# Kernel tuning notes

Measured on AMD Instinct MI355X. Metric: run time of the kernel, lower is better.

Reference implementation:

```python
import jax, jax.numpy as jnp
import numpy as np

NUM_HEADS = 16

def setup_inputs() -> dict:
    key = jax.random.key(0)
    ks = jax.random.split(key, 5)
    B, T, C = 2, 2048, 1024
    s = 0.02
    return {
        "x": jax.random.normal(ks[0], (B, T, C), dtype=jnp.float32),
        "in_w": jax.random.normal(ks[1], (3 * C, C), dtype=jnp.float32) * s,
        "in_b": jax.random.normal(ks[2], (3 * C,), dtype=jnp.float32) * s,
        "out_w": jax.random.normal(ks[3], (C, C), dtype=jnp.float32) * s,
        "out_b": jax.random.normal(ks[4], (C,), dtype=jnp.float32) * s,
    }

def reference(x, in_w, in_b, out_w, out_b):
    B, T, C = x.shape
    H = NUM_HEADS
    D = C // H
    qvk = x @ in_w.T + in_b  # (B, T, 3C)
    # einops 'b t (d k h) -> k b h t d': factor 3C as (D, 3, H), D outermost
    qvk = qvk.reshape(B, T, D, 3, H).transpose(3, 0, 4, 1, 2)  # (3, B, H, T, D)
    q, v, k = qvk[0], qvk[1], qvk[2]  # note q, v, k assignment order
    scores = jnp.einsum('bhid,bhjd->bhij', q, k) * (D ** -0.5)  # (B, H, T, T)
    causal = jnp.tril(jnp.ones((T, T), dtype=bool))
    scores = jnp.where(causal, scores, -jnp.inf)
    attn = jax.nn.softmax(scores, axis=-1)
    out = jnp.einsum('bhij,bhjd->bhid', attn, v)  # (B, H, T, D)
    out = out.transpose(0, 2, 1, 3).reshape(B, T, C)  # 'b h t d -> b t (h d)'
    return out @ out_w.T + out_b
```

## Files before the change

kernel.cpp:

```cpp
#include <hip/hip_runtime.h>


#define BB 2
#define TT 2048
#define CC 1024
#define HH 16
#define DD 64
#define MM (BB*TT)
#define N3 (3*CC)
#define BH (BB*HH)

typedef unsigned short u16;
typedef unsigned int   u32;
typedef __bf16 bf16x8 __attribute__((ext_vector_type(8)));
typedef float  f32x4  __attribute__((ext_vector_type(4)));

__device__ __forceinline__ u16 f32_to_bf16(float f) {
  u32 u = __float_as_uint(f);
  return (u16)((u + 0x7fffu + ((u >> 16) & 1u)) >> 16);
}
__device__ __forceinline__ u16 f32_to_bf16_fast(float f) {
  return (u16)((__float_as_uint(f) + 0x8000u) >> 16);
}
__device__ __forceinline__ u32 pack2_bf16(float a, float b) {
  u32 ua = __float_as_uint(a) + 0x8000u;
  u32 ub = __float_as_uint(b) + 0x8000u;
  return __builtin_amdgcn_perm(ub, ua, 0x07060302);
}

#define N4_X  (MM * CC / 4)
#define N4_W  (N3 * CC / 4)
#define N4_OW (CC * CC / 4)
__global__ __launch_bounds__(256) void cast_all(const float* __restrict__ x,
                                                const float* __restrict__ in_w,
                                                const float* __restrict__ out_w,
                                                u16* __restrict__ xb,
                                                u16* __restrict__ wb,
                                                u16* __restrict__ owb) {
  int i = blockIdx.x * 256 + threadIdx.x;
  const float* src; u16* dst; int j;
  if (i < N4_X)            { src = x;     dst = xb;  j = i; }
  else if (i < N4_X + N4_W){ src = in_w;  dst = wb;  j = i - N4_X; }
  else                     { src = out_w; dst = owb; j = i - N4_X - N4_W; }
  float4 f = reinterpret_cast<const float4*>(src)[j];
  uint2 pk;
  pk.x = (u32)f32_to_bf16(f.x) | ((u32)f32_to_bf16(f.y) << 16);
  pk.y = (u32)f32_to_bf16(f.z) | ((u32)f32_to_bf16(f.w) << 16);
  reinterpret_cast<uint2*>(dst)[j] = pk;
}

__device__ __forceinline__ void gemm_core(const u16* __restrict__ Ag,
                                          const u16* __restrict__ Bg,
                                          int K, u16* Al, u16* Bl,
                                          int m0, int n0, f32x4 acc[4][4]) {
  const int tid = threadIdx.x, lane = tid & 63, w = tid >> 6;
  const int quad = lane >> 4, colr = lane & 15;
  const int mw = (w >> 1) * 64, nw = (w & 1) * 64;
  const int srow = lane >> 3, scol = lane & 7;
  const uint4* Al4 = reinterpret_cast<const uint4*>(Al);
  const uint4* Bl4 = reinterpret_cast<const uint4*>(Bl);
  for (int kt = 0; kt < K / 64; ++kt) {
    __syncthreads();
    #pragma unroll
    for (int ii = 0; ii < 4; ++ii) {
      int inst = w * 4 + ii;
      int row = inst * 8 + srow;
      int cs = scol ^ (row & 7);
      const u16* ga = Ag + (size_t)(m0 + row) * K + kt * 64 + cs * 8;
      const u16* gb = Bg + (size_t)(n0 + row) * K + kt * 64 + cs * 8;
      __builtin_amdgcn_global_load_lds(
          (const __attribute__((address_space(1))) void*)ga,
          (__attribute__((address_space(3))) void*)(Al + inst * 512), 16, 0, 0);
      __builtin_amdgcn_global_load_lds(
          (const __attribute__((address_space(1))) void*)gb,
          (__attribute__((address_space(3))) void*)(Bl + inst * 512), 16, 0, 0);
    }
    __syncthreads();
    #pragma unroll
    for (int ks = 0; ks < 2; ++ks) {
      bf16x8 af[4], bfr[4];
      #pragma unroll
      for (int t = 0; t < 4; ++t) {
        int mrow = mw + t * 16 + colr;
        af[t]  = __builtin_bit_cast(bf16x8, Al4[mrow * 8 + ((ks * 4 + quad) ^ (mrow & 7))]);
        int nrow = nw + t * 16 + colr;
        bfr[t] = __builtin_bit_cast(bf16x8, Bl4[nrow * 8 + ((ks * 4 + quad) ^ (nrow & 7))]);
      }
      #pragma unroll
      for (int mt = 0; mt < 4; ++mt)
        #pragma unroll
        for (int nt = 0; nt < 4; ++nt)
          acc[mt][nt] = __builtin_amdgcn_mfma_f32_16x16x32_bf16(af[mt], bfr[nt], acc[mt][nt], 0, 0, 0);
    }
  }
}

__global__ __launch_bounds__(256) void gemm_qkv(const u16* __restrict__ xb,
                                                const u16* __restrict__ wb,
                                                const float* __restrict__ in_b,
                                                u16* __restrict__ Y) {
  __shared__ __align__(16) u16 Al[128 * 64];
  __shared__ __align__(16) u16 Bl[128 * 64];
  const int lane = threadIdx.x & 63, w = threadIdx.x >> 6;
  const int quad = lane >> 4, colr = lane & 15;
  const int mw = (w >> 1) * 64, nw = (w & 1) * 64;
  const int m0 = blockIdx.x * 128, n0 = blockIdx.y * 128;
  f32x4 acc[4][4];
  #pragma unroll
  for (int mt = 0; mt < 4; ++mt)
    #pragma unroll
    for (int nt = 0; nt < 4; ++nt) acc[mt][nt] = (f32x4){0.f, 0.f, 0.f, 0.f};
  gemm_core(xb, wb, CC, Al, Bl, m0, n0, acc);
  float bias[4];
  #pragma unroll
  for (int nt = 0; nt < 4; ++nt) bias[nt] = in_b[n0 + nw + nt * 16 + colr];
  #pragma unroll
  for (int mt = 0; mt < 4; ++mt)
    #pragma unroll
    for (int e = 0; e < 4; ++e) {
      int row = m0 + mw + mt * 16 + quad * 4 + e;
      #pragma unroll
      for (int nt = 0; nt < 4; ++nt)
        Y[(size_t)row * N3 + n0 + nw + nt * 16 + colr] = f32_to_bf16(acc[mt][nt][e] + bias[nt]);
    }
}

__global__ __launch_bounds__(256) void repack_qkv(const u16* __restrict__ Y,
                                                  u16* __restrict__ qkv) {
  __shared__ __align__(16) u16 Yl[N3];
  const int m = blockIdx.x, tid = threadIdx.x;
  const int b_ = m >> 11, t = m & (TT - 1);
  const uint4* Yg = reinterpret_cast<const uint4*>(Y + (size_t)m * N3);
  uint4* Yl4 = reinterpret_cast<uint4*>(Yl);
  for (int i = tid; i < N3 / 8; i += 256) Yl4[i] = Yg[i];
  __syncthreads();
  for (int it = tid; it < 768; it += 256) {
    int h = it & 15, s = (it >> 4) % 3, dg = it / 48;
    int col = s * 16 + h;
    u32 lo = (u32)Yl[(dg * 4 + 0) * 48 + col] | ((u32)Yl[(dg * 4 + 1) * 48 + col] << 16);
    u32 hi = (u32)Yl[(dg * 4 + 2) * 48 + col] | ((u32)Yl[(dg * 4 + 3) * 48 + col] << 16);
    uint2 pk; pk.x = lo; pk.y = hi;
    size_t base = (((size_t)s * BH + b_ * HH + h) * TT + t) * DD + dg * 4;
    *reinterpret_cast<uint2*>(qkv + base) = pk;
  }
}

__global__ __launch_bounds__(128) void attn_mfma(const u16* __restrict__ qkv,
                                                 u16* __restrict__ aout) {
  __shared__ __align__(16) u32   Vt[2][64 * 36];
  __shared__ __align__(16) float Pl[2 * 32 * 68];
  const int tid  = threadIdx.x;
  const int lane = tid & 63, w = tid >> 6;
  const int quad = lane >> 4, colr = lane & 15;
  const int flat = blockIdx.x;
  const int bh = (flat & 7) * 4 + (flat >> 7);
  const int pr = (flat >> 3) & 15;
  const int b_ = bh >> 4, h = bh & 15;

  const uint4* Qg4 = reinterpret_cast<const uint4*>(qkv + (size_t)bh * TT * DD);
  const uint4* Vg4 = reinterpret_cast<const uint4*>(qkv + ((size_t)BH + bh) * TT * DD);
  const uint4* Kg4 = reinterpret_cast<const uint4*>(qkv + ((size_t)2 * BH + bh) * TT * DD);
  const float4* Pl4 = reinterpret_cast<const float4*>(Pl);

  const int s_jp = tid & 31, s_half = tid >> 5;
  const int wbase = w * (32 * 68);

  for (int pass = 0; pass < 2; ++pass) {
    const int qt = pass ? (31 - pr) : pr;
    const int i0 = qt * 64;
    const int jmax = qt;

    bf16x8 qa[2][2];
    #pragma unroll
    for (int u = 0; u < 2; ++u)
      #pragma unroll
      for (int ks = 0; ks < 2; ++ks)
        qa[u][ks] = __builtin_bit_cast(bf16x8,
            Qg4[(size_t)(i0 + w * 32 + u * 16 + colr) * 8 + ks * 4 + quad]);

    f32x4 oacc[2][4];
    #pragma unroll
    for (int u = 0; u < 2; ++u)
      #pragma unroll
      for (int dt = 0; dt < 4; ++dt) oacc[u][dt] = (f32x4){0.f, 0.f, 0.f, 0.f};
    float lp[2] = {0.f, 0.f};

    uint4 va[2], vb[2];
    #pragma unroll
    for (int io = 0; io < 2; ++io) {
      va[io] = Vg4[(size_t)(2 * s_jp) * 8 + s_half + io * 4];
      vb[io] = Vg4[(size_t)(2 * s_jp + 1) * 8 + s_half + io * 4];
    }

    for (int jt = 0; jt <= jmax; ++jt) {
      const int j0 = jt * 64;
      u32* vtw = Vt[jt & 1];
      const uint4* vt4 = reinterpret_cast<const uint4*>(Vt[jt & 1]);

      uint4 kraw[4][2];
      #pragma unroll
      for (int t4 = 0; t4 < 4; ++t4)
        #pragma unroll
        for (int ks = 0; ks < 2; ++ks)
          kraw[t4][ks] = Kg4[(size_t)(j0 + t4 * 16 + colr) * 8 + ks * 4 + quad];

      #pragma unroll
      for (int io = 0; io < 2; ++io) {
        const int oc = s_half + io * 4;
        u32 aw[4] = {va[io].x, va[io].y, va[io].z, va[io].w};
        u32 bw[4] = {vb[io].x, vb[io].y, vb[io].z, vb[io].w};
        #pragma unroll
        for (int m = 0; m < 4; ++m) {
          vtw[(oc * 8 + 2 * m)     * 36 + s_jp] = __builtin_amdgcn_perm(bw[m], aw[m], 0x05040100);
          vtw[(oc * 8 + 2 * m + 1) * 36 + s_jp] = __builtin_amdgcn_perm(bw[m], aw[m], 0x07060302);
        }
      }
      if (jt < jmax) {
        int nj = j0 + 64;
        #pragma unroll
        for (int io = 0; io < 2; ++io) {
          va[io] = Vg4[(size_t)(nj + 2 * s_jp) * 8 + s_half + io * 4];
          vb[io] = Vg4[(size_t)(nj + 2 * s_jp + 1) * 8 + s_half + io * 4];
        }
      }
      __syncthreads();

      f32x4 sacc[2][4];
      #pragma unroll
      for (int u = 0; u < 2; ++u)
        #pragma unroll
        for (int t4 = 0; t4 < 4; ++t4) sacc[u][t4] = (f32x4){0.f, 0.f, 0.f, 0.f};
      #pragma unroll
      for (int t4 = 0; t4 < 4; ++t4)
        #pragma unroll
        for (int ks = 0; ks < 2; ++ks) {
          bf16x8 kb = __builtin_bit_cast(bf16x8, kraw[t4][ks]);
          #pragma unroll
          for (int u = 0; u < 2; ++u)
            sacc[u][t4] = __builtin_amdgcn_mfma_f32_16x16x32_bf16(qa[u][ks], kb, sacc[u][t4], 0, 0, 0);
        }

      const bool maskt = (jt == qt);
      #pragma unroll
      for (int u = 0; u < 2; ++u)
        #pragma unroll
        for (int t4 = 0; t4 < 4; ++t4)
          #pragma unroll
          for (int rg = 0; rg < 4; ++rg) {
            float p = __builtin_amdgcn_exp2f(sacc[u][t4][rg] * 0.18033688011112042f);
            if (maskt && (t4 * 16 + colr > w * 32 + u * 16 + quad * 4 + rg)) p = 0.f;
            Pl[wbase + (u * 16 + quad * 4 + rg) * 68 + t4 * 16 + colr] = p;
          }

      bf16x8 pa[2][2];
      #pragma unroll
      for (int u = 0; u < 2; ++u)
        #pragma unroll
        for (int ks = 0; ks < 2; ++ks) {
          int b4 = (wbase + (u * 16 + colr) * 68 + ks * 32 + quad * 8) >> 2;
          float4 f0 = Pl4[b4], f1 = Pl4[b4 + 1];
          lp[u] += ((f0.x + f0.y) + (f0.z + f0.w)) + ((f1.x + f1.y) + (f1.z + f1.w));
          uint4 up;
          up.x = pack2_bf16(f0.x, f0.y); up.y = pack2_bf16(f0.z, f0.w);
          up.z = pack2_bf16(f1.x, f1.y); up.w = pack2_bf16(f1.z, f1.w);
          pa[u][ks] = __builtin_bit_cast(bf16x8, up);
        }

      #pragma unroll
      for (int dt = 0; dt < 4; ++dt)
        #pragma unroll
        for (int ks = 0; ks < 2; ++ks) {
          bf16x8 vfr = __builtin_bit_cast(bf16x8, vt4[(dt * 16 + colr) * 9 + ks * 4 + quad]);
          #pragma unroll
          for (int u = 0; u < 2; ++u)
            oacc[u][dt] = __builtin_amdgcn_mfma_f32_16x16x32_bf16(pa[u][ks], vfr, oacc[u][dt], 0, 0, 0);
        }
    }

    #pragma unroll
    for (int u = 0; u < 2; ++u) {
      float ls = lp[u];
      ls += __shfl_xor(ls, 16);
      ls += __shfl_xor(ls, 32);
      float linv[4];
      #pragma unroll
      for (int rg = 0; rg < 4; ++rg)
        linv[rg] = 1.0f / __shfl(ls, quad * 4 + rg);
      #pragma unroll
      for (int dt = 0; dt < 4; ++dt)
        #pragma unroll
        for (int rg = 0; rg < 4; ++rg) {
          int ig = i0 + w * 32 + u * 16 + quad * 4 + rg;
          size_t off = ((size_t)(b_ * TT + ig)) * CC + h * DD + dt * 16 + colr;
          aout[off] = f32_to_bf16_fast(oacc[u][dt][rg] * linv[rg]);
        }
    }
    __syncthreads();
  }
}

__global__ __launch_bounds__(256) void gemm_out(const u16* __restrict__ ab,
                                                const u16* __restrict__ owb,
                                                const float* __restrict__ out_b,
                                                float* __restrict__ out) {
  __shared__ __align__(16) u16 Al[128 * 64];
  __shared__ __align__(16) u16 Bl[128 * 64];
  const int lane = threadIdx.x & 63, w = threadIdx.x >> 6;
  const int quad = lane >> 4, colr = lane & 15;
  const int mw = (w >> 1) * 64, nw = (w & 1) * 64;
  const int m0 = blockIdx.x * 128, n0 = blockIdx.y * 128;
  f32x4 acc[4][4];
  #pragma unroll
  for (int mt = 0; mt < 4; ++mt)
    #pragma unroll
    for (int nt = 0; nt < 4; ++nt) acc[mt][nt] = (f32x4){0.f, 0.f, 0.f, 0.f};
  gemm_core(ab, owb, CC, Al, Bl, m0, n0, acc);
  float bias[4];
  #pragma unroll
  for (int nt = 0; nt < 4; ++nt) bias[nt] = out_b[n0 + nw + nt * 16 + colr];
  #pragma unroll
  for (int mt = 0; mt < 4; ++mt)
    #pragma unroll
    for (int e = 0; e < 4; ++e) {
      int row = m0 + mw + mt * 16 + quad * 4 + e;
      #pragma unroll
      for (int nt = 0; nt < 4; ++nt)
        out[(size_t)row * CC + n0 + nw + nt * 16 + colr] = acc[mt][nt][e] + bias[nt];
    }
}

extern "C" void kernel_launch(void* const* d_in, const int* in_sizes, int n_in,
                              void* d_out, int out_size, void* d_ws, size_t ws_size,
                              hipStream_t stream) {
  const float* x     = (const float*)d_in[0];
  const float* in_w  = (const float*)d_in[1];
  const float* in_b  = (const float*)d_in[2];
  const float* out_w = (const float*)d_in[3];
  const float* out_b = (const float*)d_in[4];
  float* out = (float*)d_out;

  char* ws = (char*)d_ws;
  u16* xb  = (u16*)(ws + 0);
  u16* ab  = (u16*)(ws + 0);
  u16* wb  = (u16*)(ws + 8388608);
  u16* owb = (u16*)(ws + 14680064);
  u16* Y   = (u16*)(ws + 16777216);
  u16* qkv = (u16*)(ws + 41943040);

  cast_all<<<dim3((N4_X + N4_W + N4_OW) / 256), 256, 0, stream>>>(x, in_w, out_w, xb, wb, owb);

  gemm_qkv<<<dim3(MM / 128, N3 / 128), 256, 0, stream>>>(xb, wb, in_b, Y);
  repack_qkv<<<dim3(MM), 256, 0, stream>>>(Y, qkv);
  attn_mfma<<<dim3(512), 128, 0, stream>>>(qkv, ab);
  gemm_out<<<dim3(MM / 128, CC / 128), 256, 0, stream>>>(ab, owb, out_b, out);
}
```

Before: 226.2 us.

## Fuse QKV repack into GEMM epilogue and split attention KV range across blocks

Permutes in_w rows during the cast so the QKV GEMM writes directly in head-major layout, with the softmax scale folded into the K columns, which removes the repack kernel and the intermediate Y buffer. Attention now splits each query-tile pair's key range into four chunks across 2048 blocks and accumulates unnormalized outputs and row sums with float atomics. A new finalize kernel then normalizes the results and writes bf16. P is packed to bf16 in LDS, the Vt buffer is single-buffered, and K loads are moved inside the loop. This buys more parallelism at the cost of a large memset, atomic traffic and an extra pass.

New measurement: 246.4 us. 1.09x slower.

```diff
diff --git a/kernel.cpp b/kernel.cpp
--- a/kernel.cpp
+++ b/kernel.cpp
@@ -9,6 +9,7 @@
 #define MM (BB*TT)
 #define N3 (3*CC)
 #define BH (BB*HH)
+#define KSCALE 0.18033688011112042f
 
 typedef unsigned short u16;
 typedef unsigned int   u32;
@@ -18,9 +19,6 @@
 __device__ __forceinline__ u16 f32_to_bf16(float f) {
   u32 u = __float_as_uint(f);
   return (u16)((u + 0x7fffu + ((u >> 16) & 1u)) >> 16);
-}
-__device__ __forceinline__ u16 f32_to_bf16_fast(float f) {
-  return (u16)((__float_as_uint(f) + 0x8000u) >> 16);
 }
 __device__ __forceinline__ u32 pack2_bf16(float a, float b) {
   u32 ua = __float_as_uint(a) + 0x8000u;
@@ -38,11 +36,14 @@
                                                 u16* __restrict__ wb,
                                                 u16* __restrict__ owb) {
   int i = blockIdx.x * 256 + threadIdx.x;
-  const float* src; u16* dst; int j;
-  if (i < N4_X)            { src = x;     dst = xb;  j = i; }
-  else if (i < N4_X + N4_W){ src = in_w;  dst = wb;  j = i - N4_X; }
-  else                     { src = out_w; dst = owb; j = i - N4_X - N4_W; }
-  float4 f = reinterpret_cast<const float4*>(src)[j];
+  const float* src; u16* dst; int j; int sj;
+  if (i < N4_X)             { src = x;     dst = xb;  j = i;               sj = j; }
+  else if (i < N4_X + N4_W) { src = in_w;  dst = wb;  j = i - N4_X;
+                              int rp = j >> 8, c = j & 255;
+                              int s = rp >> 10, h = (rp >> 6) & 15, d = rp & 63;
+                              sj = (d * 48 + s * 16 + h) * 256 + c; }
+  else                      { src = out_w; dst = owb; j = i - N4_X - N4_W; sj = j; }
+  float4 f = reinterpret_cast<const float4*>(src)[sj];
   uint2 pk;
   pk.x = (u32)f32_to_bf16(f.x) | ((u32)f32_to_bf16(f.y) << 16);
   pk.y = (u32)f32_to_bf16(f.z) | ((u32)f32_to_bf16(f.w) << 16);
@@ -98,7 +99,7 @@
 __global__ __launch_bounds__(256) void gemm_qkv(const u16* __restrict__ xb,
                                                 const u16* __restrict__ wb,
                                                 const float* __restrict__ in_b,
-                                                u16* __restrict__ Y) {
+                                                u16* __restrict__ qkv) {
   __shared__ __align__(16) u16 Al[128 * 64];
   __shared__ __align__(16) u16 Bl[128 * 64];
   const int lane = threadIdx.x & 63, w = threadIdx.x >> 6;
@@ -111,64 +112,57 @@
     #pragma unroll
     for (int nt = 0; nt < 4; ++nt) acc[mt][nt] = (f32x4){0.f, 0.f, 0.f, 0.f};
   gemm_core(xb, wb, CC, Al, Bl, m0, n0, acc);
-  float bias[4];
-  #pragma unroll
-  for (int nt = 0; nt < 4; ++nt) bias[nt] = in_b[n0 + nw + nt * 16 + colr];
-  #pragma unroll
-  for (int mt = 0; mt < 4; ++mt)
-    #pragma unroll
-    for (int e = 0; e < 4; ++e) {
-      int row = m0 + mw + mt * 16 + quad * 4 + e;
-      #pragma unroll
-      for (int nt = 0; nt < 4; ++nt)
-        Y[(size_t)row * N3 + n0 + nw + nt * 16 + colr] = f32_to_bf16(acc[mt][nt][e] + bias[nt]);
-    }
-}
-
-__global__ __launch_bounds__(256) void repack_qkv(const u16* __restrict__ Y,
-                                                  u16* __restrict__ qkv) {
-  __shared__ __align__(16) u16 Yl[N3];
-  const int m = blockIdx.x, tid = threadIdx.x;
-  const int b_ = m >> 11, t = m & (TT - 1);
-  const uint4* Yg = reinterpret_cast<const uint4*>(Y + (size_t)m * N3);
-  uint4* Yl4 = reinterpret_cast<uint4*>(Yl);
-  for (int i = tid; i < N3 / 8; i += 256) Yl4[i] = Yg[i];
-  __syncthreads();
-  for (int it = tid; it < 768; it += 256) {
-    int h = it & 15, s = (it >> 4) % 3, dg = it / 48;
-    int col = s * 16 + h;
-    u32 lo = (u32)Yl[(dg * 4 + 0) * 48 + col] | ((u32)Yl[(dg * 4 + 1) * 48 + col] << 16);
-    u32 hi = (u32)Yl[(dg * 4 + 2) * 48 + col] | ((u32)Yl[(dg * 4 + 3) * 48 + col] << 16);
-    uint2 pk; pk.x = lo; pk.y = hi;
-    size_t base = (((size_t)s * BH + b_ * HH + h) * TT + t) * DD + dg * 4;
-    *reinterpret_cast<uint2*>(qkv + base) = pk;
+  const int b_ = m0 >> 11;
+  #pragma unroll
+  for (int nt = 0; nt < 4; ++nt) {
+    int np = n0 + nw + nt * 16 + colr;
+    int s = np >> 10, h = (np >> 6) & 15, d = np & 63;
+    float bias = in_b[d * 48 + s * 16 + h];
+    float sc = (s == 2) ? KSCALE : 1.0f;
+    u16* base = qkv + ((size_t)(s * BH + b_ * HH + h) * TT) * DD + d;
+    #pragma unroll
+    for (int mt = 0; mt < 4; ++mt)
+      #pragma unroll
+      for (int e = 0; e < 4; ++e) {
+        int t = (m0 + mw + mt * 16 + quad * 4 + e) & (TT - 1);
+        base[(size_t)t * DD] = f32_to_bf16((acc[mt][nt][e] + bias) * sc);
+      }
   }
 }
 
-__global__ __launch_bounds__(128) void attn_mfma(const u16* __restrict__ qkv,
-                                                 u16* __restrict__ aout) {
-  __shared__ __align__(16) u32   Vt[2][64 * 36];
-  __shared__ __align__(16) float Pl[2 * 32 * 68];
+__global__ __launch_bounds__(128, 4) void attn_mfma(const u16* __restrict__ qkv,
+                                                    float* __restrict__ po,
+                                                    float* __restrict__ pl) {
+  __shared__ __align__(16) u32 Vt[64 * 36];
+  __shared__ __align__(16) u32 Pl[2 * 32 * 36];
   const int tid  = threadIdx.x;
   const int lane = tid & 63, w = tid >> 6;
   const int quad = lane >> 4, colr = lane & 15;
-  const int flat = blockIdx.x;
-  const int bh = (flat & 7) * 4 + (flat >> 7);
-  const int pr = (flat >> 3) & 15;
-  const int b_ = bh >> 4, h = bh & 15;
+  const int f = blockIdx.x;
+  const int qq = (f >> 3) & 3;
+  const int pr = (f >> 5) & 15;
+  const int bh = (f & 7) * 4 + (f >> 9);
 
   const uint4* Qg4 = reinterpret_cast<const uint4*>(qkv + (size_t)bh * TT * DD);
   const uint4* Vg4 = reinterpret_cast<const uint4*>(qkv + ((size_t)BH + bh) * TT * DD);
   const uint4* Kg4 = reinterpret_cast<const uint4*>(qkv + ((size_t)2 * BH + bh) * TT * DD);
-  const float4* Pl4 = reinterpret_cast<const float4*>(Pl);
+  const uint4* Vt4 = reinterpret_cast<const uint4*>(Vt);
+  const uint4* Pl4 = reinterpret_cast<const uint4*>(Pl);
 
   const int s_jp = tid & 31, s_half = tid >> 5;
-  const int wbase = w * (32 * 68);
-
-  for (int pass = 0; pass < 2; ++pass) {
-    const int qt = pass ? (31 - pr) : pr;
+  const int wb32 = w * (32 * 36);
+
+  const int vlo = (qq == 0) ? 0 : (qq * 8 + 1);
+  const int vhi = qq * 8 + 8;
+  int sqt[2], sjlo[2], sjhi[2], nseg = 0;
+  if (vlo <= pr) { sqt[nseg] = pr; sjlo[nseg] = vlo; sjhi[nseg] = vhi < pr ? vhi : pr; ++nseg; }
+  if (vhi > pr)  { sqt[nseg] = 31 - pr;
+                   int lo = (vlo > pr + 1 ? vlo : pr + 1) - (pr + 1);
+                   sjlo[nseg] = lo; sjhi[nseg] = vhi - (pr + 1); ++nseg; }
+
+  for (int sg = 0; sg < nseg; ++sg) {
+    const int qt = sqt[sg], jlo = sjlo[sg], jhi = sjhi[sg];
     const int i0 = qt * 64;
-    const int jmax = qt;
 
     bf16x8 qa[2][2];
     #pragma unroll
@@ -188,22 +182,13 @@
     uint4 va[2], vb[2];
     #pragma unroll
     for (int io = 0; io < 2; ++io) {
-      va[io] = Vg4[(size_t)(2 * s_jp) * 8 + s_half + io * 4];
-      vb[io] = Vg4[(size_t)(2 * s_jp + 1) * 8 + s_half + io * 4];
-    }
-
-    for (int jt = 0; jt <= jmax; ++jt) {
+      va[io] = Vg4[(size_t)(jlo * 64 + 2 * s_jp) * 8 + s_half + io * 4];
+      vb[io] = Vg4[(size_t)(jlo * 64 + 2 * s_jp + 1) * 8 + s_half + io * 4];
+    }
+
+    for (int jt = jlo; jt <= jhi; ++jt) {
       const int j0 = jt * 64;
-      u32* vtw = Vt[jt & 1];
-      const uint4* vt4 = reinterpret_cast<const uint4*>(Vt[jt & 1]);
-
-      uint4 kraw[4][2];
-      #pragma unroll
-      for (int t4 = 0; t4 < 4; ++t4)
-        #pragma unroll
-        for (int ks = 0; ks < 2; ++ks)
-          kraw[t4][ks] = Kg4[(size_t)(j0 + t4 * 16 + colr) * 8 + ks * 4 + quad];
-
+      __syncthreads();
       #pragma unroll
       for (int io = 0; io < 2; ++io) {
         const int oc = s_half + io * 4;
@@ -211,11 +196,11 @@
         u32 bw[4] = {vb[io].x, vb[io].y, vb[io].z, vb[io].w};
         #pragma unroll
         for (int m = 0; m < 4; ++m) {
-          vtw[(oc * 8 + 2 * m)     * 36 + s_jp] = __builtin_amdgcn_perm(bw[m], aw[m], 0x05040100);
-          vtw[(oc * 8 + 2 * m + 1) * 36 + s_jp] = __builtin_amdgcn_perm(bw[m], aw[m], 0x07060302);
+          Vt[(oc * 8 + 2 * m)     * 36 + s_jp] = __builtin_amdgcn_perm(bw[m], aw[m], 0x05040100);
+          Vt[(oc * 8 + 2 * m + 1) * 36 + s_jp] = __builtin_amdgcn_perm(bw[m], aw[m], 0x07060302);
         }
       }
-      if (jt < jmax) {
+      if (jt < jhi) {
         int nj = j0 + 64;
         #pragma unroll
         for (int io = 0; io < 2; ++io) {
@@ -231,71 +216,108 @@
         #pragma unroll
         for (int t4 = 0; t4 < 4; ++t4) sacc[u][t4] = (f32x4){0.f, 0.f, 0.f, 0.f};
       #pragma unroll
-      for (int t4 = 0; t4 < 4; ++t4)
-        #pragma unroll
-        for (int ks = 0; ks < 2; ++ks) {
-          bf16x8 kb = __builtin_bit_cast(bf16x8, kraw[t4][ks]);
+      for (int ks = 0; ks < 2; ++ks) {
+        uint4 kk[4];
+        #pragma unroll
+        for (int t4 = 0; t4 < 4; ++t4)
+          kk[t4] = Kg4[(size_t)(j0 + t4 * 16 + colr) * 8 + ks * 4 + quad];
+        #pragma unroll
+        for (int t4 = 0; t4 < 4; ++t4) {
+          bf16x8 kb = __builtin_bit_cast(bf16x8, kk[t4]);
           #pragma unroll
           for (int u = 0; u < 2; ++u)
-            sacc[u][t4] = __builtin_amdgcn_mfma_f32_16x16x32_bf16(qa[u][ks], kb, sacc[u][t4], 0, 0, 0);
+            sacc[u][t4] = __builtin_amdgcn_mfma_f32_16x16x32_bf16(kb, qa[u][ks], sacc[u][t4], 0, 0, 0);
         }
-
-      const bool maskt = (jt == qt);
-      #pragma unroll
-      for (int u = 0; u < 2; ++u)
-        #pragma unroll
-        for (int t4 = 0; t4 < 4; ++t4)
+      }
+
+      if (jt == qt) {
+        #pragma unroll
+        for (int u = 0; u < 2; ++u) {
+          const int qv = w * 32 + u * 16 + colr;
           #pragma unroll
-          for (int rg = 0; rg < 4; ++rg) {
-            float p = __builtin_amdgcn_exp2f(sacc[u][t4][rg] * 0.18033688011112042f);
-            if (maskt && (t4 * 16 + colr > w * 32 + u * 16 + quad * 4 + rg)) p = 0.f;
-            Pl[wbase + (u * 16 + quad * 4 + rg) * 68 + t4 * 16 + colr] = p;
+          for (int t4 = 0; t4 < 4; ++t4) {
+            float p0 = __builtin_amdgcn_exp2f(sacc[u][t4][0]);
+            float p1 = __builtin_amdgcn_exp2f(sacc[u][t4][1]);
+            float p2 = __builtin_amdgcn_exp2f(sacc[u][t4][2]);
+            float p3 = __builtin_amdgcn_exp2f(sacc[u][t4][3]);
+            int jb = t4 * 16 + quad * 4;
+            if (jb + 0 > qv) p0 = 0.f;
+            if (jb + 1 > qv) p1 = 0.f;
+            if (jb + 2 > qv) p2 = 0.f;
+            if (jb + 3 > qv) p3 = 0.f;
+            lp[u] += (p0 + p1) + (p2 + p3);
+            uint2 pw; pw.x = pack2_bf16(p0, p1); pw.y = pack2_bf16(p2, p3);
+            *reinterpret_cast<uint2*>(Pl + wb32 + (u * 16 + colr) * 36 + t4 * 8 + quad * 2) = pw;
           }
-
-      bf16x8 pa[2][2];
-      #pragma unroll
-      for (int u = 0; u < 2; ++u)
-        #pragma unroll
-        for (int ks = 0; ks < 2; ++ks) {
-          int b4 = (wbase + (u * 16 + colr) * 68 + ks * 32 + quad * 8) >> 2;
-          float4 f0 = Pl4[b4], f1 = Pl4[b4 + 1];
-          lp[u] += ((f0.x + f0.y) + (f0.z + f0.w)) + ((f1.x + f1.y) + (f1.z + f1.w));
-          uint4 up;
-          up.x = pack2_bf16(f0.x, f0.y); up.y = pack2_bf16(f0.z, f0.w);
-          up.z = pack2_bf16(f1.x, f1.y); up.w = pack2_bf16(f1.z, f1.w);
-          pa[u][ks] = __builtin_bit_cast(bf16x8, up);
         }
-
-      #pragma unroll
-      for (int dt = 0; dt < 4; ++dt)
-        #pragma unroll
-        for (int ks = 0; ks < 2; ++ks) {
-          bf16x8 vfr = __builtin_bit_cast(bf16x8, vt4[(dt * 16 + colr) * 9 + ks * 4 + quad]);
+      } else {
+        #pragma unroll
+        for (int u = 0; u < 2; ++u)
           #pragma unroll
-          for (int u = 0; u < 2; ++u)
-            oacc[u][dt] = __builtin_amdgcn_mfma_f32_16x16x32_bf16(pa[u][ks], vfr, oacc[u][dt], 0, 0, 0);
-        }
-    }
-
+          for (int t4 = 0; t4 < 4; ++t4) {
+            float p0 = __builtin_amdgcn_exp2f(sacc[u][t4][0]);
+            float p1 = __builtin_amdgcn_exp2f(sacc[u][t4][1]);
+            float p2 = __builtin_amdgcn_exp2f(sacc[u][t4][2]);
+            float p3 = __builtin_amdgcn_exp2f(sacc[u][t4][3]);
+            lp[u] += (p0 + p1) + (p2 + p3);
+            uint2 pw; pw.x = pack2_bf16(p0, p1); pw.y = pack2_bf16(p2, p3);
+            *reinterpret_cast<uint2*>(Pl + wb32 + (u * 16 + colr) * 36 + t4 * 8 + quad * 2) = pw;
+          }
+      }
+
+      #pragma unroll
+      for (int u = 0; u < 2; ++u) {
+        bf16x8 pa[2];
+        #pragma unroll
+        for (int ks = 0; ks < 2; ++ks)
+          pa[ks] = __builtin_bit_cast(bf16x8,
+              Pl4[(wb32 + (u * 16 + colr) * 36 + ks * 16 + quad * 4) >> 2]);
+        #pragma unroll
+        for (int dt = 0; dt < 4; ++dt)
+          #pragma unroll
+          for (int ks = 0; ks < 2; ++ks) {
+            bf16x8 vfr = __builtin_bit_cast(bf16x8, Vt4[(dt * 16 + colr) * 9 + ks * 4 + quad]);
+            oacc[u][dt] = __builtin_amdgcn_mfma_f32_16x16x32_bf16(pa[ks], vfr, oacc[u][dt], 0, 0, 0);
+          }
+      }
+    }
+
+    const int slot = bh * 32 + qt;
+    float* ob = po + (size_t)slot * 4096;
     #pragma unroll
     for (int u = 0; u < 2; ++u) {
       float ls = lp[u];
       ls += __shfl_xor(ls, 16);
       ls += __shfl_xor(ls, 32);
-      float linv[4];
-      #pragma unroll
-      for (int rg = 0; rg < 4; ++rg)
-        linv[rg] = 1.0f / __shfl(ls, quad * 4 + rg);
+      if (quad == 0) atomicAdd(&pl[slot * 64 + w * 32 + u * 16 + colr], ls);
       #pragma unroll
       for (int dt = 0; dt < 4; ++dt)
         #pragma unroll
-        for (int rg = 0; rg < 4; ++rg) {
-          int ig = i0 + w * 32 + u * 16 + quad * 4 + rg;
-          size_t off = ((size_t)(b_ * TT + ig)) * CC + h * DD + dt * 16 + colr;
-          aout[off] = f32_to_bf16_fast(oacc[u][dt][rg] * linv[rg]);
-        }
-    }
-    __syncthreads();
+        for (int rg = 0; rg < 4; ++rg)
+          atomicAdd(&ob[(w * 32 + u * 16 + quad * 4 + rg) * 64 + dt * 16 + colr],
+                    oacc[u][dt][rg]);
+    }
+  }
+}
+
+__global__ __launch_bounds__(256) void attn_finalize(const float* __restrict__ po,
+                                                     const float* __restrict__ pl,
+                                                     u16* __restrict__ ab) {
+  const int slot = blockIdx.x;
+  const int bh = slot >> 5, qt = slot & 31;
+  const int b_ = bh >> 4, h = bh & 15;
+  const int t = threadIdx.x;
+  const int r = t >> 2, dq = t & 3;
+  const float4* o4 = reinterpret_cast<const float4*>(po + (size_t)slot * 4096 + r * 64 + dq * 16);
+  float inv = 1.0f / pl[slot * 64 + r];
+  u16* dst = ab + ((size_t)(b_ * TT + qt * 64 + r)) * CC + h * DD + dq * 16;
+  #pragma unroll
+  for (int c = 0; c < 4; ++c) {
+    float4 a = o4[c];
+    uint2 pk;
+    pk.x = pack2_bf16(a.x * inv, a.y * inv);
+    pk.y = pack2_bf16(a.z * inv, a.w * inv);
+    *reinterpret_cast<uint2*>(dst + c * 4) = pk;
   }
 }
 
@@ -340,17 +362,19 @@
   float* out = (float*)d_out;
 
   char* ws = (char*)d_ws;
-  u16* xb  = (u16*)(ws + 0);
-  u16* ab  = (u16*)(ws + 0);
-  u16* wb  = (u16*)(ws + 8388608);
-  u16* owb = (u16*)(ws + 14680064);
-  u16* Y   = (u16*)(ws + 16777216);
-  u16* qkv = (u16*)(ws + 41943040);
-
+  u16* xb   = (u16*)(ws + 0);
+  u16* ab   = (u16*)(ws + 0);
+  u16* wb   = (u16*)(ws + 8388608);
+  u16* owb  = (u16*)(ws + 14680064);
+  float* po = (float*)(ws + 16777216);
+  float* pl = (float*)(ws + 16777216 + 16777216);
+  u16* qkv  = (u16*)(ws + 41943040);
+
+  hipMemsetAsync(po, 0, 16777216 + 262144, stream);
   cast_all<<<dim3((N4_X + N4_W + N4_OW) / 256), 256, 0, stream>>>(x, in_w, out_w, xb, wb, owb);
 
-  gemm_qkv<<<dim3(MM / 128, N3 / 128), 256, 0, stream>>>(xb, wb, in_b, Y);
-  repack_qkv<<<dim3(MM), 256, 0, stream>>>(Y, qkv);
-  attn_mfma<<<dim3(512), 128, 0, stream>>>(qkv, ab);
+  gemm_qkv<<<dim3(MM / 128, N3 / 128), 256, 0, stream>>>(xb, wb, in_b, qkv);
+  attn_mfma<<<dim3(2048), 128, 0, stream>>>(qkv, po, pl);
+  attn_finalize<<<dim3(1024), 256, 0, stream>>>(po, pl, ab);
   gemm_out<<<dim3(MM / 128, CC / 128), 256, 0, stream>>>(ab, owb, out_b, out);
 }
```
